# Optimization experiments

Hardware: AMD Instinct MI355X
Metric: run time of the kernel (lower is better)

Reference implementation:

```python
import jax, jax.numpy as jnp
import numpy as np

N = 32768
LATENT = 2
HID = 100
STEPS = 100

swish = jax.nn.swish


def setup_inputs() -> dict:
    key = jax.random.key(0)
    ks = jax.random.split(key, 12)

    def w(k, shape):
        fan_in = shape[0]
        return (jax.random.normal(k, shape) / np.sqrt(fan_in)).astype(jnp.float32)

    return {
        "x": jax.random.normal(ks[0], (N, 3), dtype=jnp.float32),
        # encoder: 3 -> 100 -> 100 -> (mu: 2, log_t: 1)
        "We1": w(ks[1], (3, HID)), "be1": jnp.zeros((HID,), jnp.float32),
        "We2": w(ks[2], (HID, HID)), "be2": jnp.zeros((HID,), jnp.float32),
        "Wmu": w(ks[3], (HID, LATENT)), "bmu": jnp.zeros((LATENT,), jnp.float32),
        "Wlt": w(ks[4], (HID, 1)), "blt": jnp.zeros((1,), jnp.float32),
        # decoder: 2 -> 100 -> (mu: 3, log_sigma: 3)
        "Wd1": w(ks[5], (LATENT, HID)), "bd1": jnp.zeros((HID,), jnp.float32),
        "Wdmu": w(ks[6], (HID, 3)), "bdmu": jnp.zeros((3,), jnp.float32),
        "Wds": w(ks[7], (HID, 3)), "bds": jnp.zeros((3,), jnp.float32),
        # prior layer biases
        "b_muz": jnp.zeros((LATENT,), jnp.float32),
        "b_ltz": jnp.zeros((1,), jnp.float32),
        # standard-normal noise for the 100-step SDE (dW = sqrt(dt) * noise)
        "noise": jax.random.normal(ks[8], (STEPS, N, LATENT), dtype=jnp.float32),
    }


def reference(x, We1, be1, We2, be2, Wmu, bmu, Wlt, blt,
              Wd1, bd1, Wdmu, bdmu, Wds, bds, b_muz, b_ltz, noise):
    x = x.astype(jnp.float32)

    # ---- decoder heads on a single latent point z: (LATENT,) ----
    def dec_mu(z):
        return swish(z @ Wd1 + bd1) @ Wdmu + bdmu      # (3,)

    def dec_ls(z):
        return swish(z @ Wd1 + bd1) @ Wds + bds        # (3,)

    def G(z):  # pullback metric, (LATENT, LATENT)
        Jmu = jax.jacfwd(dec_mu)(z)   # (3, LATENT)
        Jsg = jax.jacfwd(dec_ls)(z)   # (3, LATENT)
        return Jmu.T @ Jmu + Jsg.T @ Jsg

    def step_one(z, dW):  # one Euler-Maruyama step for one point
        g = G(z)
        ginv = jnp.linalg.inv(g)
        Dg = jax.jacfwd(G)(z)         # (LATENT, LATENT, LATENT): dG[k,m]/dz_l
        Chris = 0.5 * (jnp.einsum('im,kml->ikl', ginv, Dg)
                       + jnp.einsum('im,lmk->ikl', ginv, Dg)
                       - jnp.einsum('im,klm->ikl', ginv, Dg))
        det = 0.5 * jnp.einsum('jk,ijk->i', ginv, Chris)
        stoch = ginv @ dW
        return (z + det + stoch).astype(jnp.float32)

    # ---- encoder ----
    h = swish(x @ We1 + be1)
    h = swish(h @ We2 + be2)
    mu_zx = h @ Wmu + bmu            # (N, LATENT)
    log_t_zx = h @ Wlt + blt         # (N, 1)

    # ---- Riemannian Brownian-motion sampling (Local) ----
    t = jnp.exp(2.0 * log_t_zx)[:, 0]        # (N,)
    dt = t / STEPS                            # (N,), constant over steps
    dW = jnp.sqrt(dt)[None, :, None] * noise  # (STEPS, N, LATENT)

    def scan_step(z, dW_t):
        return jax.vmap(step_one)(z, dW_t), None

    z, _ = jax.lax.scan(scan_step, mu_zx, dW)

    # ---- prior + decoder outputs ----
    mu_z = b_muz * jnp.ones_like(z)
    log_t_z = b_ltz * jnp.ones((z.shape[0], 1), z.dtype)
    hz = swish(z @ Wd1 + bd1)
    mu_xz = hz @ Wdmu + bdmu
    log_sigma_xz = hz @ Wds + bds

    return (z, mu_xz, log_sigma_xz, mu_zx, log_t_zx, mu_z, log_t_z)
```

## Files before the change

### kernel.cpp

```cpp
#include <hip/hip_runtime.h>

#define N_PTS 32768
#define HID   100
#define STEPS 100
#define NPAIR 52
#define LPP   13

#define OFF_Z     0
#define OFF_MUXZ  65536
#define OFF_LSXZ  163840
#define OFF_MUZX  262144
#define OFF_LTZX  327680
#define OFF_MUZ   360448
#define OFF_LTZ   425984

typedef float v2f __attribute__((ext_vector_type(2)));
typedef float v4f __attribute__((ext_vector_type(4)));

#if __has_builtin(__builtin_elementwise_fma)
#define FMA2(a, b, c) __builtin_elementwise_fma((a), (b), (c))
#else
#define FMA2(a, b, c) ((a) * (b) + (c))
#endif
#define LOv(q) __builtin_shufflevector((q), (q), 0, 1)
#define HIv(q) __builtin_shufflevector((q), (q), 2, 3)

__device__ __forceinline__ v2f splat(float x) { v2f r; r.x = x; r.y = x; return r; }

__device__ __forceinline__ float qreduce(float v) {
  v += __int_as_float(__builtin_amdgcn_update_dpp(0, __float_as_int(v), 0xB1, 0xF, 0xF, true));
  v += __int_as_float(__builtin_amdgcn_update_dpp(0, __float_as_int(v), 0x4E, 0xF, 0xF, true));
  return v;
}
__device__ __forceinline__ float hqreduce(v2f v) { return qreduce(v.x + v.y); }

template<int NP>
__device__ __forceinline__ void enc_chunk(
    int ob, float x0, float x1, float x2,
    const float* __restrict__ We1, const float* __restrict__ be1,
    const float* __restrict__ We2, const float* __restrict__ be2,
    const float* __restrict__ Wmu, const float* __restrict__ Wlt,
    float& m0, float& m1, float& lt)
{
  v2f acc2[NP];
  #pragma unroll
  for (int i = 0; i < NP; ++i) acc2[i] = splat(0.f);

  #pragma unroll 2
  for (int k = 0; k < HID; k += 2) {
    const v2f w0 = *(const v2f*)(We1 + k);
    const v2f w1 = *(const v2f*)(We1 + HID + k);
    const v2f w2 = *(const v2f*)(We1 + 2*HID + k);
    const v2f bb = *(const v2f*)(be1 + k);
    v2f aP = FMA2(splat(x0), w0, FMA2(splat(x1), w1, FMA2(splat(x2), w2, bb)));
    const float e0 = __expf(-aP.x), e1 = __expf(-aP.y);
    const float s0 = 1.f / (1.f + e0), s1 = 1.f / (1.f + e1);
    const v2f hh0 = splat(aP.x * s0);
    const v2f hh1 = splat(aP.y * s1);
    const v2f* r0 = (const v2f*)(We2 + k*HID + ob);
    const v2f* r1 = (const v2f*)(We2 + (k+1)*HID + ob);
    #pragma unroll
    for (int oo = 0; oo < NP; ++oo) {
      v2f tacc = FMA2(hh0, r0[oo], acc2[oo]);
      acc2[oo] = FMA2(hh1, r1[oo], tacc);
    }
  }

  m0 = 0.f; m1 = 0.f; lt = 0.f;
  #pragma unroll
  for (int oo = 0; oo < NP; ++oo) {
    #pragma unroll
    for (int h = 0; h < 2; ++h) {
      const int o = ob + 2*oo + h;
      float a   = (h ? acc2[oo].y : acc2[oo].x) + be2[o];
      float sig = 1.f / (1.f + __expf(-a));
      float h2  = a * sig;
      m0 = fmaf(h2, Wmu[o*2+0], m0);
      m1 = fmaf(h2, Wmu[o*2+1], m1);
      lt = fmaf(h2, Wlt[o],     lt);
    }
  }
}

__global__ __launch_bounds__(256, 2) void vaebm_kernel(
    const float* __restrict__ x,
    const float* __restrict__ We1, const float* __restrict__ be1,
    const float* __restrict__ We2, const float* __restrict__ be2,
    const float* __restrict__ Wmu, const float* __restrict__ bmu,
    const float* __restrict__ Wlt, const float* __restrict__ blt,
    const float* __restrict__ Wd1,  const float* __restrict__ bd1,
    const float* __restrict__ Wdmu, const float* __restrict__ bdmu,
    const float* __restrict__ Wds,  const float* __restrict__ bds,
    const float* __restrict__ b_muz, const float* __restrict__ b_ltz,
    const float* __restrict__ noise,
    float* __restrict__ out)
{
  __shared__ __align__(16) float wrec[NPAIR * 24];
  __shared__ float red[4][64][3];
  __shared__ float zlds[64][3];

  const int tid = threadIdx.x;

  for (int idx = tid; idx < NPAIR * 24; idx += 256) {
    const int pr = idx / 24, f = idx - pr * 24;
    const int j  = pr * 2 + (f & 1);
    const int g  = f >> 1;
    float v = 0.f;
    if (j < HID) {
      const float w0 = Wd1[j], w1 = Wd1[HID + j];
      switch (g) {
        case 0:  v = w0; break;
        case 1:  v = w1; break;
        case 2:  v = bd1[j]; break;
        case 3:  v = w1 * w1; break;
        case 4:  v = w0 * w0; break;
        case 5:  v = w0 * w1; break;
        case 6:  v = Wdmu[j*3+0]; break;
        case 7:  v = Wds [j*3+0]; break;
        case 8:  v = Wdmu[j*3+1]; break;
        case 9:  v = Wds [j*3+1]; break;
        case 10: v = Wdmu[j*3+2]; break;
        default: v = Wds [j*3+2]; break;
      }
    }
    wrec[idx] = v;
  }

  const int w  = tid >> 6;
  const int pb = tid & 63;
  const int p  = blockIdx.x * 64 + pb;

  const float x0 = x[p*3+0], x1 = x[p*3+1], x2 = x[p*3+2];

  float m0, m1, lt;
  if (w < 2) enc_chunk<13>(w * 26,            x0, x1, x2, We1, be1, We2, be2, Wmu, Wlt, m0, m1, lt);
  else       enc_chunk<12>(52 + (w - 2) * 24, x0, x1, x2, We1, be1, We2, be2, Wmu, Wlt, m0, m1, lt);

  red[w][pb][0] = m0; red[w][pb][1] = m1; red[w][pb][2] = lt;
  __syncthreads();
  if (w == 0) {
    m0 += red[1][pb][0] + red[2][pb][0] + red[3][pb][0] + bmu[0];
    m1 += red[1][pb][1] + red[2][pb][1] + red[3][pb][1] + bmu[1];
    lt += red[1][pb][2] + red[2][pb][2] + red[3][pb][2] + blt[0];
    out[OFF_MUZX + p*2+0] = m0;
    out[OFF_MUZX + p*2+1] = m1;
    out[OFF_LTZX + p]     = lt;
    out[OFF_MUZ  + p*2+0] = b_muz[0];
    out[OFF_MUZ  + p*2+1] = b_muz[1];
    out[OFF_LTZ  + p]     = b_ltz[0];
    zlds[pb][0] = m0; zlds[pb][1] = m1; zlds[pb][2] = lt;
  }
  __syncthreads();

  const int l     = tid & 3;
  const int pt    = tid >> 2;
  const int pg    = blockIdx.x * 64 + pt;
  const int pbase = l * LPP;
  const v4f* __restrict__ Rq = (const v4f*)wrec;

  float z0 = zlds[pt][0];
  float z1 = zlds[pt][1];
  const float sdt = __expf(zlds[pt][2]) * 0.1f;

  const float2* __restrict__ noise2 = (const float2*)noise;

  for (int step = 0; step < STEPS; ++step) {
    const float2 nz = noise2[(size_t)step * N_PTS + pg];

    v2f Jm[3][2], Js[3][2], Km[3][3], Ks[3][3];
    #pragma unroll
    for (int o = 0; o < 3; ++o) {
      Jm[o][0]=splat(0.f); Jm[o][1]=splat(0.f);
      Js[o][0]=splat(0.f); Js[o][1]=splat(0.f);
      Km[o][0]=splat(0.f); Km[o][1]=splat(0.f); Km[o][2]=splat(0.f);
      Ks[o][0]=splat(0.f); Ks[o][1]=splat(0.f); Ks[o][2]=splat(0.f);
    }
    const v2f z0P = splat(z0), z1P = splat(z1);

    const v4f* R = Rq + pbase * 6;
    #pragma unroll 4
    for (int t = 0; t < LPP; ++t, R += 6) {
      const v4f A  = R[0];
      const v4f B  = R[1];
      const v4f Cq = R[2];
      const v4f M0 = R[3], M1 = R[4], M2 = R[5];
      const v2f W0P  = LOv(A),  W1P  = HIv(A);
      const v2f bP   = LOv(B),  W11P = HIv(B);
      const v2f W00P = LOv(Cq), W01P = HIv(Cq);

      v2f aP = FMA2(z0P, W0P, FMA2(z1P, W1P, bP));
      v2f eP;   eP.x   = __expf(-aP.x);               eP.y   = __expf(-aP.y);
      v2f dP = splat(1.f) + eP;
      v2f sigP; sigP.x = __builtin_amdgcn_rcpf(dP.x); sigP.y = __builtin_amdgcn_rcpf(dP.y);
      const v2f ppP  = FMA2(-sigP, sigP, sigP);
      const v2f uP   = FMA2(aP, ppP, sigP);
      const v2f w2sP = FMA2(splat(-2.f), sigP, splat(1.f));
      const v2f u2P  = FMA2(uP, w2sP, sigP);
      const v2f c0  = uP  * W0P,  c1  = uP  * W1P;
      const v2f q00 = u2P * W00P, q01 = u2P * W01P, q11 = u2P * W11P;

      const v2f mP0 = LOv(M0), mP1 = LOv(M1), mP2 = LOv(M2);
      const v2f sP0 = HIv(M0), sP1 = HIv(M1), sP2 = HIv(M2);

      Jm[0][0] = FMA2(c0,  mP0, Jm[0][0]);  Jm[0][1] = FMA2(c1,  mP0, Jm[0][1]);
      Js[0][0] = FMA2(c0,  sP0, Js[0][0]);  Js[0][1] = FMA2(c1,  sP0, Js[0][1]);
      Km[0][0] = FMA2(q00, mP0, Km[0][0]);  Km[0][1] = FMA2(q01, mP0, Km[0][1]);
      Km[0][2] = FMA2(q11, mP0, Km[0][2]);
      Ks[0][0] = FMA2(q00, sP0, Ks[0][0]);  Ks[0][1] = FMA2(q01, sP0, Ks[0][1]);
      Ks[0][2] = FMA2(q11, sP0, Ks[0][2]);

      Jm[1][0] = FMA2(c0,  mP1, Jm[1][0]);  Jm[1][1] = FMA2(c1,  mP1, Jm[1][1]);
      Js[1][0] = FMA2(c0,  sP1, Js[1][0]);  Js[1][1] = FMA2(c1,  sP1, Js[1][1]);
      Km[1][0] = FMA2(q00, mP1, Km[1][0]);  Km[1][1] = FMA2(q01, mP1, Km[1][1]);
      Km[1][2] = FMA2(q11, mP1, Km[1][2]);
      Ks[1][0] = FMA2(q00, sP1, Ks[1][0]);  Ks[1][1] = FMA2(q01, sP1, Ks[1][1]);
      Ks[1][2] = FMA2(q11, sP1, Ks[1][2]);

      Jm[2][0] = FMA2(c0,  mP2, Jm[2][0]);  Jm[2][1] = FMA2(c1,  mP2, Jm[2][1]);
      Js[2][0] = FMA2(c0,  sP2, Js[2][0]);  Js[2][1] = FMA2(c1,  sP2, Js[2][1]);
      Km[2][0] = FMA2(q00, mP2, Km[2][0]);  Km[2][1] = FMA2(q01, mP2, Km[2][1]);
      Km[2][2] = FMA2(q11, mP2, Km[2][2]);
      Ks[2][0] = FMA2(q00, sP2, Ks[2][0]);  Ks[2][1] = FMA2(q01, sP2, Ks[2][1]);
      Ks[2][2] = FMA2(q11, sP2, Ks[2][2]);
    }

    float JmS[3][2], JsS[3][2], KmS[3][3], KsS[3][3];
    #pragma unroll
    for (int o = 0; o < 3; ++o) {
      JmS[o][0]=hqreduce(Jm[o][0]); JmS[o][1]=hqreduce(Jm[o][1]);
      JsS[o][0]=hqreduce(Js[o][0]); JsS[o][1]=hqreduce(Js[o][1]);
      KmS[o][0]=hqreduce(Km[o][0]); KmS[o][1]=hqreduce(Km[o][1]); KmS[o][2]=hqreduce(Km[o][2]);
      KsS[o][0]=hqreduce(Ks[o][0]); KsS[o][1]=hqreduce(Ks[o][1]); KsS[o][2]=hqreduce(Ks[o][2]);
    }

    float G00=0.f, G01=0.f, G11=0.f;
    #pragma unroll
    for (int o = 0; o < 3; ++o) {
      G00 += JmS[o][0]*JmS[o][0] + JsS[o][0]*JsS[o][0];
      G01 += JmS[o][0]*JmS[o][1] + JsS[o][0]*JsS[o][1];
      G11 += JmS[o][1]*JmS[o][1] + JsS[o][1]*JsS[o][1];
    }
    float D00=0.f, D01=0.f, D10=0.f, D11=0.f, D20=0.f, D21=0.f;
    #pragma unroll
    for (int o = 0; o < 3; ++o) {
      D00 += 2.f*(KmS[o][0]*JmS[o][0] + KsS[o][0]*JsS[o][0]);
      D01 += 2.f*(KmS[o][1]*JmS[o][0] + KsS[o][1]*JsS[o][0]);
      D10 += KmS[o][0]*JmS[o][1] + JmS[o][0]*KmS[o][1] + KsS[o][0]*JsS[o][1] + JsS[o][0]*KsS[o][1];
      D11 += KmS[o][1]*JmS[o][1] + JmS[o][0]*KmS[o][2] + KsS[o][1]*JsS[o][1] + JsS[o][0]*KsS[o][2];
      D20 += 2.f*(KmS[o][1]*JmS[o][1] + KsS[o][1]*JsS[o][1]);
      D21 += 2.f*(KmS[o][2]*JmS[o][1] + KsS[o][2]*JsS[o][1]);
    }
    const float det = fmaf(G00, G11, -G01*G01);
    const float id  = __builtin_amdgcn_rcpf(det);
    const float i00 = G11*id, i01 = -G01*id, i11 = G00*id;
    const float S0 = fmaf(i00, D00, fmaf(i01, D01 + D10, i11 * D11));
    const float S1 = fmaf(i00, D10, fmaf(i01, D11 + D20, i11 * D21));
    const float i01d = i01 + i01;
    const float P0 = fmaf(i00, D00, fmaf(i01d, D10, i11 * D20));
    const float P1 = fmaf(i00, D01, fmaf(i01d, D11, i11 * D21));
    const float R0 = fmaf(0.5f, S0, -0.25f * P0);
    const float R1 = fmaf(0.5f, S1, -0.25f * P1);
    const float dr0 = fmaf(i00, R0, i01 * R1);
    const float dr1 = fmaf(i01, R0, i11 * R1);

    const float dw0 = sdt*nz.x, dw1 = sdt*nz.y;
    z0 += dr0 + i00*dw0 + i01*dw1;
    z1 += dr1 + i01*dw0 + i11*dw1;
  }

  v2f MSm[3], MSs[3];
  #pragma unroll
  for (int o = 0; o < 3; ++o) { MSm[o] = splat(0.f); MSs[o] = splat(0.f); }
  const v2f zf0 = splat(z0), zf1 = splat(z1);
  {
    const v4f* R = Rq + pbase * 6;
    #pragma unroll 2
    for (int t = 0; t < LPP; ++t, R += 6) {
      const v4f A  = R[0];
      const v4f B  = R[1];
      const v4f M0 = R[3], M1 = R[4], M2 = R[5];
      v2f aP = FMA2(zf0, LOv(A), FMA2(zf1, HIv(A), LOv(B)));
      v2f eP;   eP.x   = __expf(-aP.x);               eP.y   = __expf(-aP.y);
      v2f dP = splat(1.f) + eP;
      v2f sigP; sigP.x = __builtin_amdgcn_rcpf(dP.x); sigP.y = __builtin_amdgcn_rcpf(dP.y);
      const v2f hP = aP * sigP;
      MSm[0] = FMA2(hP, LOv(M0), MSm[0]);  MSs[0] = FMA2(hP, HIv(M0), MSs[0]);
      MSm[1] = FMA2(hP, LOv(M1), MSm[1]);  MSs[1] = FMA2(hP, HIv(M1), MSs[1]);
      MSm[2] = FMA2(hP, LOv(M2), MSm[2]);  MSs[2] = FMA2(hP, HIv(M2), MSs[2]);
    }
  }
  float mu[3], ls[3];
  #pragma unroll
  for (int o = 0; o < 3; ++o) { mu[o] = hqreduce(MSm[o]); ls[o] = hqreduce(MSs[o]); }

  if (l == 0) {
    out[OFF_Z + pg*2+0] = z0;
    out[OFF_Z + pg*2+1] = z1;
    #pragma unroll
    for (int o = 0; o < 3; ++o) {
      out[OFF_MUXZ + pg*3 + o] = mu[o] + bdmu[o];
      out[OFF_LSXZ + pg*3 + o] = ls[o] + bds[o];
    }
  }
}

extern "C" void kernel_launch(void* const* d_in, const int* in_sizes, int n_in,
                              void* d_out, int out_size, void* d_ws, size_t ws_size,
                              hipStream_t stream) {
  (void)in_sizes; (void)n_in; (void)d_ws; (void)ws_size; (void)out_size;
  const float* x    = (const float*)d_in[0];
  const float* We1  = (const float*)d_in[1];
  const float* be1  = (const float*)d_in[2];
  const float* We2  = (const float*)d_in[3];
  const float* be2  = (const float*)d_in[4];
  const float* Wmu  = (const float*)d_in[5];
  const float* bmu  = (const float*)d_in[6];
  const float* Wlt  = (const float*)d_in[7];
  const float* blt  = (const float*)d_in[8];
  const float* Wd1  = (const float*)d_in[9];
  const float* bd1  = (const float*)d_in[10];
  const float* Wdmu = (const float*)d_in[11];
  const float* bdmu = (const float*)d_in[12];
  const float* Wds  = (const float*)d_in[13];
  const float* bds  = (const float*)d_in[14];
  const float* bmz  = (const float*)d_in[15];
  const float* blz  = (const float*)d_in[16];
  const float* noise= (const float*)d_in[17];
  float* out = (float*)d_out;

  vaebm_kernel<<<512, 256, 0, stream>>>(x, We1, be1, We2, be2, Wmu, bmu, Wlt, blt,
                                        Wd1, bd1, Wdmu, bdmu, Wds, bds,
                                        bmz, blz, noise, out);
}
```

Baseline: 574.0 us.

## Split encoder into its own kernel and process two points per thread in SDE

Separates the encoder into a standalone kernel that writes mu and log_t to the output buffer. A second SDE kernel then reads them back and has each thread integrate two points at once, which halves the grid to 256 blocks. This lets each LDS weight load be reused across two points and gives more independent work to hide latency. In exchange it doubles the accumulator register count (launch bounds drop to 1 block/SM), leaves fewer waves per CU, and adds a kernel launch plus a global round trip.

Result: slower. 635.5 us (+10.7%).

```diff
diff --git a/kernel.cpp b/kernel.cpp
--- a/kernel.cpp
+++ b/kernel.cpp
@@ -82,25 +82,159 @@
   }
 }
 
-__global__ __launch_bounds__(256, 2) void vaebm_kernel(
+__global__ __launch_bounds__(256, 2) void enc_kernel(
     const float* __restrict__ x,
     const float* __restrict__ We1, const float* __restrict__ be1,
     const float* __restrict__ We2, const float* __restrict__ be2,
     const float* __restrict__ Wmu, const float* __restrict__ bmu,
     const float* __restrict__ Wlt, const float* __restrict__ blt,
+    const float* __restrict__ b_muz, const float* __restrict__ b_ltz,
+    float* __restrict__ out)
+{
+  const int tid = threadIdx.x;
+  const int w   = tid >> 6;
+  const int pb  = tid & 63;
+  const int p   = blockIdx.x * 64 + pb;
+
+  const float x0 = x[p*3+0], x1 = x[p*3+1], x2 = x[p*3+2];
+
+  float m0, m1, lt;
+  if (w < 2) enc_chunk<13>(w * 26,            x0, x1, x2, We1, be1, We2, be2, Wmu, Wlt, m0, m1, lt);
+  else       enc_chunk<12>(52 + (w - 2) * 24, x0, x1, x2, We1, be1, We2, be2, Wmu, Wlt, m0, m1, lt);
+
+  __shared__ float red[4][64][3];
+  red[w][pb][0] = m0; red[w][pb][1] = m1; red[w][pb][2] = lt;
+  __syncthreads();
+  if (w == 0) {
+    m0 += red[1][pb][0] + red[2][pb][0] + red[3][pb][0] + bmu[0];
+    m1 += red[1][pb][1] + red[2][pb][1] + red[3][pb][1] + bmu[1];
+    lt += red[1][pb][2] + red[2][pb][2] + red[3][pb][2] + blt[0];
+    out[OFF_MUZX + p*2+0] = m0;
+    out[OFF_MUZX + p*2+1] = m1;
+    out[OFF_LTZX + p]     = lt;
+    out[OFF_MUZ  + p*2+0] = b_muz[0];
+    out[OFF_MUZ  + p*2+1] = b_muz[1];
+    out[OFF_LTZ  + p]     = b_ltz[0];
+  }
+}
+
+struct Acc {
+  v2f Jm00, Jm01, Jm10, Jm11, Jm20, Jm21;
+  v2f Js00, Js01, Js10, Js11, Js20, Js21;
+  v2f Km00, Km01, Km02, Km10, Km11, Km12, Km20, Km21, Km22;
+  v2f Ks00, Ks01, Ks02, Ks10, Ks11, Ks12, Ks20, Ks21, Ks22;
+};
+
+__device__ __forceinline__ void acc_zero(Acc& A) {
+  const v2f z = splat(0.f);
+  A.Jm00=z; A.Jm01=z; A.Jm10=z; A.Jm11=z; A.Jm20=z; A.Jm21=z;
+  A.Js00=z; A.Js01=z; A.Js10=z; A.Js11=z; A.Js20=z; A.Js21=z;
+  A.Km00=z; A.Km01=z; A.Km02=z; A.Km10=z; A.Km11=z; A.Km12=z;
+  A.Km20=z; A.Km21=z; A.Km22=z;
+  A.Ks00=z; A.Ks01=z; A.Ks02=z; A.Ks10=z; A.Ks11=z; A.Ks12=z;
+  A.Ks20=z; A.Ks21=z; A.Ks22=z;
+}
+
+__device__ __forceinline__ void pair_update(
+    float z0, float z1,
+    v2f W0P, v2f W1P, v2f bP, v2f W11P, v2f W00P, v2f W01P,
+    v2f mP0, v2f mP1, v2f mP2, v2f sP0, v2f sP1, v2f sP2,
+    Acc& A)
+{
+  const v2f z0P = splat(z0), z1P = splat(z1);
+  v2f aP = FMA2(z0P, W0P, FMA2(z1P, W1P, bP));
+  v2f eP;   eP.x   = __expf(-aP.x);               eP.y   = __expf(-aP.y);
+  v2f dP = splat(1.f) + eP;
+  v2f sigP; sigP.x = __builtin_amdgcn_rcpf(dP.x); sigP.y = __builtin_amdgcn_rcpf(dP.y);
+  const v2f ppP  = FMA2(-sigP, sigP, sigP);
+  const v2f uP   = FMA2(aP, ppP, sigP);
+  const v2f w2sP = FMA2(splat(-2.f), sigP, splat(1.f));
+  const v2f u2P  = FMA2(uP, w2sP, sigP);
+  const v2f c0  = uP  * W0P,  c1  = uP  * W1P;
+  const v2f q00 = u2P * W00P, q01 = u2P * W01P, q11 = u2P * W11P;
+
+  A.Jm00 = FMA2(c0,  mP0, A.Jm00);  A.Jm01 = FMA2(c1,  mP0, A.Jm01);
+  A.Js00 = FMA2(c0,  sP0, A.Js00);  A.Js01 = FMA2(c1,  sP0, A.Js01);
+  A.Km00 = FMA2(q00, mP0, A.Km00);  A.Km01 = FMA2(q01, mP0, A.Km01);
+  A.Km02 = FMA2(q11, mP0, A.Km02);
+  A.Ks00 = FMA2(q00, sP0, A.Ks00);  A.Ks01 = FMA2(q01, sP0, A.Ks01);
+  A.Ks02 = FMA2(q11, sP0, A.Ks02);
+
+  A.Jm10 = FMA2(c0,  mP1, A.Jm10);  A.Jm11 = FMA2(c1,  mP1, A.Jm11);
+  A.Js10 = FMA2(c0,  sP1, A.Js10);  A.Js11 = FMA2(c1,  sP1, A.Js11);
+  A.Km10 = FMA2(q00, mP1, A.Km10);  A.Km11 = FMA2(q01, mP1, A.Km11);
+  A.Km12 = FMA2(q11, mP1, A.Km12);
+  A.Ks10 = FMA2(q00, sP1, A.Ks10);  A.Ks11 = FMA2(q01, sP1, A.Ks11);
+  A.Ks12 = FMA2(q11, sP1, A.Ks12);
+
+  A.Jm20 = FMA2(c0,  mP2, A.Jm20);  A.Jm21 = FMA2(c1,  mP2, A.Jm21);
+  A.Js20 = FMA2(c0,  sP2, A.Js20);  A.Js21 = FMA2(c1,  sP2, A.Js21);
+  A.Km20 = FMA2(q00, mP2, A.Km20);  A.Km21 = FMA2(q01, mP2, A.Km21);
+  A.Km22 = FMA2(q11, mP2, A.Km22);
+  A.Ks20 = FMA2(q00, sP2, A.Ks20);  A.Ks21 = FMA2(q01, sP2, A.Ks21);
+  A.Ks22 = FMA2(q11, sP2, A.Ks22);
+}
+
+__device__ __forceinline__ void tail_update(Acc& A, float& z0, float& z1,
+                                            float sdt, float nx, float ny)
+{
+  float JmS[3][2] = {{hqreduce(A.Jm00), hqreduce(A.Jm01)},
+                     {hqreduce(A.Jm10), hqreduce(A.Jm11)},
+                     {hqreduce(A.Jm20), hqreduce(A.Jm21)}};
+  float JsS[3][2] = {{hqreduce(A.Js00), hqreduce(A.Js01)},
+                     {hqreduce(A.Js10), hqreduce(A.Js11)},
+                     {hqreduce(A.Js20), hqreduce(A.Js21)}};
+  float KmS[3][3] = {{hqreduce(A.Km00), hqreduce(A.Km01), hqreduce(A.Km02)},
+                     {hqreduce(A.Km10), hqreduce(A.Km11), hqreduce(A.Km12)},
+                     {hqreduce(A.Km20), hqreduce(A.Km21), hqreduce(A.Km22)}};
+  float KsS[3][3] = {{hqreduce(A.Ks00), hqreduce(A.Ks01), hqreduce(A.Ks02)},
+                     {hqreduce(A.Ks10), hqreduce(A.Ks11), hqreduce(A.Ks12)},
+                     {hqreduce(A.Ks20), hqreduce(A.Ks21), hqreduce(A.Ks22)}};
+
+  float G00=0.f, G01=0.f, G11=0.f;
+  #pragma unroll
+  for (int o = 0; o < 3; ++o) {
+    G00 += JmS[o][0]*JmS[o][0] + JsS[o][0]*JsS[o][0];
+    G01 += JmS[o][0]*JmS[o][1] + JsS[o][0]*JsS[o][1];
+    G11 += JmS[o][1]*JmS[o][1] + JsS[o][1]*JsS[o][1];
+  }
+  float D00=0.f, D01=0.f, D10=0.f, D11=0.f, D20=0.f, D21=0.f;
+  #pragma unroll
+  for (int o = 0; o < 3; ++o) {
+    D00 += 2.f*(KmS[o][0]*JmS[o][0] + KsS[o][0]*JsS[o][0]);
+    D01 += 2.f*(KmS[o][1]*JmS[o][0] + KsS[o][1]*JsS[o][0]);
+    D10 += KmS[o][0]*JmS[o][1] + JmS[o][0]*KmS[o][1] + KsS[o][0]*JsS[o][1] + JsS[o][0]*KsS[o][1];
+    D11 += KmS[o][1]*JmS[o][1] + JmS[o][0]*KmS[o][2] + KsS[o][1]*JsS[o][1] + JsS[o][0]*KsS[o][2];
+    D20 += 2.f*(KmS[o][1]*JmS[o][1] + KsS[o][1]*JsS[o][1]);
+    D21 += 2.f*(KmS[o][2]*JmS[o][1] + KsS[o][2]*JsS[o][1]);
+  }
+  const float det = fmaf(G00, G11, -G01*G01);
+  const float id  = __builtin_amdgcn_rcpf(det);
+  const float i00 = G11*id, i01 = -G01*id, i11 = G00*id;
+  const float S0 = fmaf(i00, D00, fmaf(i01, D01 + D10, i11 * D11));
+  const float S1 = fmaf(i00, D10, fmaf(i01, D11 + D20, i11 * D21));
+  const float i01d = i01 + i01;
+  const float P0 = fmaf(i00, D00, fmaf(i01d, D10, i11 * D20));
+  const float P1 = fmaf(i00, D01, fmaf(i01d, D11, i11 * D21));
+  const float R0 = fmaf(0.5f, S0, -0.25f * P0);
+  const float R1 = fmaf(0.5f, S1, -0.25f * P1);
+  const float dr0 = fmaf(i00, R0, i01 * R1);
+  const float dr1 = fmaf(i01, R0, i11 * R1);
+
+  const float dw0 = sdt*nx, dw1 = sdt*ny;
+  z0 += dr0 + i00*dw0 + i01*dw1;
+  z1 += dr1 + i01*dw0 + i11*dw1;
+}
+
+__global__ __launch_bounds__(256, 1) void sde_kernel(
     const float* __restrict__ Wd1,  const float* __restrict__ bd1,
     const float* __restrict__ Wdmu, const float* __restrict__ bdmu,
     const float* __restrict__ Wds,  const float* __restrict__ bds,
-    const float* __restrict__ b_muz, const float* __restrict__ b_ltz,
     const float* __restrict__ noise,
     float* __restrict__ out)
 {
   __shared__ __align__(16) float wrec[NPAIR * 24];
-  __shared__ float red[4][64][3];
-  __shared__ float zlds[64][3];
-
   const int tid = threadIdx.x;
-
   for (int idx = tid; idx < NPAIR * 24; idx += 256) {
     const int pr = idx / 24, f = idx - pr * 24;
     const int j  = pr * 2 + (f & 1);
@@ -125,60 +259,30 @@
     }
     wrec[idx] = v;
   }
-
-  const int w  = tid >> 6;
-  const int pb = tid & 63;
-  const int p  = blockIdx.x * 64 + pb;
-
-  const float x0 = x[p*3+0], x1 = x[p*3+1], x2 = x[p*3+2];
-
-  float m0, m1, lt;
-  if (w < 2) enc_chunk<13>(w * 26,            x0, x1, x2, We1, be1, We2, be2, Wmu, Wlt, m0, m1, lt);
-  else       enc_chunk<12>(52 + (w - 2) * 24, x0, x1, x2, We1, be1, We2, be2, Wmu, Wlt, m0, m1, lt);
-
-  red[w][pb][0] = m0; red[w][pb][1] = m1; red[w][pb][2] = lt;
   __syncthreads();
-  if (w == 0) {
-    m0 += red[1][pb][0] + red[2][pb][0] + red[3][pb][0] + bmu[0];
-    m1 += red[1][pb][1] + red[2][pb][1] + red[3][pb][1] + bmu[1];
-    lt += red[1][pb][2] + red[2][pb][2] + red[3][pb][2] + blt[0];
-    out[OFF_MUZX + p*2+0] = m0;
-    out[OFF_MUZX + p*2+1] = m1;
-    out[OFF_LTZX + p]     = lt;
-    out[OFF_MUZ  + p*2+0] = b_muz[0];
-    out[OFF_MUZ  + p*2+1] = b_muz[1];
-    out[OFF_LTZ  + p]     = b_ltz[0];
-    zlds[pb][0] = m0; zlds[pb][1] = m1; zlds[pb][2] = lt;
-  }
-  __syncthreads();
 
   const int l     = tid & 3;
-  const int pt    = tid >> 2;
-  const int pg    = blockIdx.x * 64 + pt;
+  const int q     = tid >> 2;
+  const int pA    = blockIdx.x * 128 + q * 2;
+  const int pB    = pA + 1;
   const int pbase = l * LPP;
   const v4f* __restrict__ Rq = (const v4f*)wrec;
 
-  float z0 = zlds[pt][0];
-  float z1 = zlds[pt][1];
-  const float sdt = __expf(zlds[pt][2]) * 0.1f;
-
-  const float2* __restrict__ noise2 = (const float2*)noise;
+  float zA0 = out[OFF_MUZX + pA*2+0], zA1 = out[OFF_MUZX + pA*2+1];
+  float zB0 = out[OFF_MUZX + pB*2+0], zB1 = out[OFF_MUZX + pB*2+1];
+  const float sdtA = __expf(out[OFF_LTZX + pA]) * 0.1f;
+  const float sdtB = __expf(out[OFF_LTZX + pB]) * 0.1f;
+
+  const float4* __restrict__ noise4 = (const float4*)noise;
 
   for (int step = 0; step < STEPS; ++step) {
-    const float2 nz = noise2[(size_t)step * N_PTS + pg];
-
-    v2f Jm[3][2], Js[3][2], Km[3][3], Ks[3][3];
-    #pragma unroll
-    for (int o = 0; o < 3; ++o) {
-      Jm[o][0]=splat(0.f); Jm[o][1]=splat(0.f);
-      Js[o][0]=splat(0.f); Js[o][1]=splat(0.f);
-      Km[o][0]=splat(0.f); Km[o][1]=splat(0.f); Km[o][2]=splat(0.f);
-      Ks[o][0]=splat(0.f); Ks[o][1]=splat(0.f); Ks[o][2]=splat(0.f);
-    }
-    const v2f z0P = splat(z0), z1P = splat(z1);
+    const float4 nzAB = noise4[((size_t)step * N_PTS + pA) >> 1];
+
+    Acc accA, accB;
+    acc_zero(accA); acc_zero(accB);
 
     const v4f* R = Rq + pbase * 6;
-    #pragma unroll 4
+    #pragma unroll 2
     for (int t = 0; t < LPP; ++t, R += 6) {
       const v4f A  = R[0];
       const v4f B  = R[1];
@@ -187,91 +291,27 @@
       const v2f W0P  = LOv(A),  W1P  = HIv(A);
       const v2f bP   = LOv(B),  W11P = HIv(B);
       const v2f W00P = LOv(Cq), W01P = HIv(Cq);
-
-      v2f aP = FMA2(z0P, W0P, FMA2(z1P, W1P, bP));
-      v2f eP;   eP.x   = __expf(-aP.x);               eP.y   = __expf(-aP.y);
-      v2f dP = splat(1.f) + eP;
-      v2f sigP; sigP.x = __builtin_amdgcn_rcpf(dP.x); sigP.y = __builtin_amdgcn_rcpf(dP.y);
-      const v2f ppP  = FMA2(-sigP, sigP, sigP);
-      const v2f uP   = FMA2(aP, ppP, sigP);
-      const v2f w2sP = FMA2(splat(-2.f), sigP, splat(1.f));
-      const v2f u2P  = FMA2(uP, w2sP, sigP);
-      const v2f c0  = uP  * W0P,  c1  = uP  * W1P;
-      const v2f q00 = u2P * W00P, q01 = u2P * W01P, q11 = u2P * W11P;
-
       const v2f mP0 = LOv(M0), mP1 = LOv(M1), mP2 = LOv(M2);
       const v2f sP0 = HIv(M0), sP1 = HIv(M1), sP2 = HIv(M2);
 
-      Jm[0][0] = FMA2(c0,  mP0, Jm[0][0]);  Jm[0][1] = FMA2(c1,  mP0, Jm[0][1]);
-      Js[0][0] = FMA2(c0,  sP0, Js[0][0]);  Js[0][1] = FMA2(c1,  sP0, Js[0][1]);
-      Km[0][0] = FMA2(q00, mP0, Km[0][0]);  Km[0][1] = FMA2(q01, mP0, Km[0][1]);
-      Km[0][2] = FMA2(q11, mP0, Km[0][2]);
-      Ks[0][0] = FMA2(q00, sP0, Ks[0][0]);  Ks[0][1] = FMA2(q01, sP0, Ks[0][1]);
-      Ks[0][2] = FMA2(q11, sP0, Ks[0][2]);
-
-      Jm[1][0] = FMA2(c0,  mP1, Jm[1][0]);  Jm[1][1] = FMA2(c1,  mP1, Jm[1][1]);
-      Js[1][0] = FMA2(c0,  sP1, Js[1][0]);  Js[1][1] = FMA2(c1,  sP1, Js[1][1]);
-      Km[1][0] = FMA2(q00, mP1, Km[1][0]);  Km[1][1] = FMA2(q01, mP1, Km[1][1]);
-      Km[1][2] = FMA2(q11, mP1, Km[1][2]);
-      Ks[1][0] = FMA2(q00, sP1, Ks[1][0]);  Ks[1][1] = FMA2(q01, sP1, Ks[1][1]);
-      Ks[1][2] = FMA2(q11, sP1, Ks[1][2]);
-
-      Jm[2][0] = FMA2(c0,  mP2, Jm[2][0]);  Jm[2][1] = FMA2(c1,  mP2, Jm[2][1]);
-      Js[2][0] = FMA2(c0,  sP2, Js[2][0]);  Js[2][1] = FMA2(c1,  sP2, Js[2][1]);
-      Km[2][0] = FMA2(q00, mP2, Km[2][0]);  Km[2][1] = FMA2(q01, mP2, Km[2][1]);
-      Km[2][2] = FMA2(q11, mP2, Km[2][2]);
-      Ks[2][0] = FMA2(q00, sP2, Ks[2][0]);  Ks[2][1] = FMA2(q01, sP2, Ks[2][1]);
-      Ks[2][2] = FMA2(q11, sP2, Ks[2][2]);
-    }
-
-    float JmS[3][2], JsS[3][2], KmS[3][3], KsS[3][3];
-    #pragma unroll
-    for (int o = 0; o < 3; ++o) {
-      JmS[o][0]=hqreduce(Jm[o][0]); JmS[o][1]=hqreduce(Jm[o][1]);
-      JsS[o][0]=hqreduce(Js[o][0]); JsS[o][1]=hqreduce(Js[o][1]);
-      KmS[o][0]=hqreduce(Km[o][0]); KmS[o][1]=hqreduce(Km[o][1]); KmS[o][2]=hqreduce(Km[o][2]);
-      KsS[o][0]=hqreduce(Ks[o][0]); KsS[o][1]=hqreduce(Ks[o][1]); KsS[o][2]=hqreduce(Ks[o][2]);
-    }
-
-    float G00=0.f, G01=0.f, G11=0.f;
-    #pragma unroll
-    for (int o = 0; o < 3; ++o) {
-      G00 += JmS[o][0]*JmS[o][0] + JsS[o][0]*JsS[o][0];
-      G01 += JmS[o][0]*JmS[o][1] + JsS[o][0]*JsS[o][1];
-      G11 += JmS[o][1]*JmS[o][1] + JsS[o][1]*JsS[o][1];
-    }
-    float D00=0.f, D01=0.f, D10=0.f, D11=0.f, D20=0.f, D21=0.f;
-    #pragma unroll
-    for (int o = 0; o < 3; ++o) {
-      D00 += 2.f*(KmS[o][0]*JmS[o][0] + KsS[o][0]*JsS[o][0]);
-      D01 += 2.f*(KmS[o][1]*JmS[o][0] + KsS[o][1]*JsS[o][0]);
-      D10 += KmS[o][0]*JmS[o][1] + JmS[o][0]*KmS[o][1] + KsS[o][0]*JsS[o][1] + JsS[o][0]*KsS[o][1];
-      D11 += KmS[o][1]*JmS[o][1] + JmS[o][0]*KmS[o][2] + KsS[o][1]*JsS[o][1] + JsS[o][0]*KsS[o][2];
-      D20 += 2.f*(KmS[o][1]*JmS[o][1] + KsS[o][1]*JsS[o][1]);
-      D21 += 2.f*(KmS[o][2]*JmS[o][1] + KsS[o][2]*JsS[o][1]);
-    }
-    const float det = fmaf(G00, G11, -G01*G01);
-    const float id  = __builtin_amdgcn_rcpf(det);
-    const float i00 = G11*id, i01 = -G01*id, i11 = G00*id;
-    const float S0 = fmaf(i00, D00, fmaf(i01, D01 + D10, i11 * D11));
-    const float S1 = fmaf(i00, D10, fmaf(i01, D11 + D20, i11 * D21));
-    const float i01d = i01 + i01;
-    const float P0 = fmaf(i00, D00, fmaf(i01d, D10, i11 * D20));
-    const float P1 = fmaf(i00, D01, fmaf(i01d, D11, i11 * D21));
-    const float R0 = fmaf(0.5f, S0, -0.25f * P0);
-    const float R1 = fmaf(0.5f, S1, -0.25f * P1);
-    const float dr0 = fmaf(i00, R0, i01 * R1);
-    const float dr1 = fmaf(i01, R0, i11 * R1);
-
-    const float dw0 = sdt*nz.x, dw1 = sdt*nz.y;
-    z0 += dr0 + i00*dw0 + i01*dw1;
-    z1 += dr1 + i01*dw0 + i11*dw1;
-  }
-
-  v2f MSm[3], MSs[3];
-  #pragma unroll
-  for (int o = 0; o < 3; ++o) { MSm[o] = splat(0.f); MSs[o] = splat(0.f); }
-  const v2f zf0 = splat(z0), zf1 = splat(z1);
+      pair_update(zA0, zA1, W0P, W1P, bP, W11P, W00P, W01P,
+                  mP0, mP1, mP2, sP0, sP1, sP2, accA);
+      pair_update(zB0, zB1, W0P, W1P, bP, W11P, W00P, W01P,
+                  mP0, mP1, mP2, sP0, sP1, sP2, accB);
+    }
+
+    tail_update(accA, zA0, zA1, sdtA, nzAB.x, nzAB.y);
+    tail_update(accB, zB0, zB1, sdtB, nzAB.z, nzAB.w);
+  }
+
+  v2f MSmA[3], MSsA[3], MSmB[3], MSsB[3];
+  #pragma unroll
+  for (int o = 0; o < 3; ++o) {
+    MSmA[o] = splat(0.f); MSsA[o] = splat(0.f);
+    MSmB[o] = splat(0.f); MSsB[o] = splat(0.f);
+  }
+  const v2f zA0P = splat(zA0), zA1P = splat(zA1);
+  const v2f zB0P = splat(zB0), zB1P = splat(zB1);
   {
     const v4f* R = Rq + pbase * 6;
     #pragma unroll 2
@@ -279,27 +319,46 @@
       const v4f A  = R[0];
       const v4f B  = R[1];
       const v4f M0 = R[3], M1 = R[4], M2 = R[5];
-      v2f aP = FMA2(zf0, LOv(A), FMA2(zf1, HIv(A), LOv(B)));
-      v2f eP;   eP.x   = __expf(-aP.x);               eP.y   = __expf(-aP.y);
-      v2f dP = splat(1.f) + eP;
-      v2f sigP; sigP.x = __builtin_amdgcn_rcpf(dP.x); sigP.y = __builtin_amdgcn_rcpf(dP.y);
-      const v2f hP = aP * sigP;
-      MSm[0] = FMA2(hP, LOv(M0), MSm[0]);  MSs[0] = FMA2(hP, HIv(M0), MSs[0]);
-      MSm[1] = FMA2(hP, LOv(M1), MSm[1]);  MSs[1] = FMA2(hP, HIv(M1), MSs[1]);
-      MSm[2] = FMA2(hP, LOv(M2), MSm[2]);  MSs[2] = FMA2(hP, HIv(M2), MSs[2]);
-    }
-  }
-  float mu[3], ls[3];
-  #pragma unroll
-  for (int o = 0; o < 3; ++o) { mu[o] = hqreduce(MSm[o]); ls[o] = hqreduce(MSs[o]); }
+      const v2f W0P = LOv(A), W1P = HIv(A), bP = LOv(B);
+      const v2f mP0 = LOv(M0), mP1 = LOv(M1), mP2 = LOv(M2);
+      const v2f sP0 = HIv(M0), sP1 = HIv(M1), sP2 = HIv(M2);
+
+      v2f aA = FMA2(zA0P, W0P, FMA2(zA1P, W1P, bP));
+      v2f eA;   eA.x   = __expf(-aA.x);               eA.y   = __expf(-aA.y);
+      v2f dA = splat(1.f) + eA;
+      v2f sgA; sgA.x = __builtin_amdgcn_rcpf(dA.x);   sgA.y = __builtin_amdgcn_rcpf(dA.y);
+      const v2f hA = aA * sgA;
+
+      v2f aB = FMA2(zB0P, W0P, FMA2(zB1P, W1P, bP));
+      v2f eB;   eB.x   = __expf(-aB.x);               eB.y   = __expf(-aB.y);
+      v2f dB = splat(1.f) + eB;
+      v2f sgB; sgB.x = __builtin_amdgcn_rcpf(dB.x);   sgB.y = __builtin_amdgcn_rcpf(dB.y);
+      const v2f hB = aB * sgB;
+
+      MSmA[0] = FMA2(hA, mP0, MSmA[0]);  MSsA[0] = FMA2(hA, sP0, MSsA[0]);
+      MSmA[1] = FMA2(hA, mP1, MSmA[1]);  MSsA[1] = FMA2(hA, sP1, MSsA[1]);
+      MSmA[2] = FMA2(hA, mP2, MSmA[2]);  MSsA[2] = FMA2(hA, sP2, MSsA[2]);
+      MSmB[0] = FMA2(hB, mP0, MSmB[0]);  MSsB[0] = FMA2(hB, sP0, MSsB[0]);
+      MSmB[1] = FMA2(hB, mP1, MSmB[1]);  MSsB[1] = FMA2(hB, sP1, MSsB[1]);
+      MSmB[2] = FMA2(hB, mP2, MSmB[2]);  MSsB[2] = FMA2(hB, sP2, MSsB[2]);
+    }
+  }
+  float muA[3], lsA[3], muB[3], lsB[3];
+  #pragma unroll
+  for (int o = 0; o < 3; ++o) {
+    muA[o] = hqreduce(MSmA[o]); lsA[o] = hqreduce(MSsA[o]);
+    muB[o] = hqreduce(MSmB[o]); lsB[o] = hqreduce(MSsB[o]);
+  }
 
   if (l == 0) {
-    out[OFF_Z + pg*2+0] = z0;
-    out[OFF_Z + pg*2+1] = z1;
+    out[OFF_Z + pA*2+0] = zA0;  out[OFF_Z + pA*2+1] = zA1;
+    out[OFF_Z + pB*2+0] = zB0;  out[OFF_Z + pB*2+1] = zB1;
     #pragma unroll
     for (int o = 0; o < 3; ++o) {
-      out[OFF_MUXZ + pg*3 + o] = mu[o] + bdmu[o];
-      out[OFF_LSXZ + pg*3 + o] = ls[o] + bds[o];
+      out[OFF_MUXZ + pA*3 + o] = muA[o] + bdmu[o];
+      out[OFF_LSXZ + pA*3 + o] = lsA[o] + bds[o];
+      out[OFF_MUXZ + pB*3 + o] = muB[o] + bdmu[o];
+      out[OFF_LSXZ + pB*3 + o] = lsB[o] + bds[o];
     }
   }
 }
@@ -328,7 +387,7 @@
   const float* noise= (const float*)d_in[17];
   float* out = (float*)d_out;
 
-  vaebm_kernel<<<512, 256, 0, stream>>>(x, We1, be1, We2, be2, Wmu, bmu, Wlt, blt,
-                                        Wd1, bd1, Wdmu, bdmu, Wds, bds,
-                                        bmz, blz, noise, out);
-}
+  enc_kernel<<<512, 256, 0, stream>>>(x, We1, be1, We2, be2, Wmu, bmu, Wlt, blt,
+                                      bmz, blz, out);
+  sde_kernel<<<256, 256, 0, stream>>>(Wd1, bd1, Wdmu, bdmu, Wds, bds, noise, out);
+}
```
